# Kernel tuning notes

Hardware: AMD Instinct MI355X
Metric: run time of the kernel (lower is better)

The kernel has to match this reference:

```python
import jax, jax.numpy as jnp
import numpy as np

INPUTS = 6
GROUPS = 10
EPS = 1e-4

def setup_inputs() -> dict:
    key = jax.random.key(0)
    k1, k2, k3 = jax.random.split(key, 3)
    B = 1048576
    out = jax.random.normal(k1, (B, GROUPS * INPUTS), dtype=jnp.float32)
    # 10 Linear(6,1) layers stacked: W [10,6], b [10]
    bound = 1.0 / np.sqrt(INPUTS)
    W = jax.random.uniform(k2, (GROUPS, INPUTS), jnp.float32, -bound, bound)
    b = jax.random.uniform(k3, (GROUPS,), jnp.float32, -bound, bound)
    gamma = jnp.ones((GROUPS,), jnp.float32)
    beta = jnp.zeros((GROUPS,), jnp.float32)
    return {"out": out, "W": W, "b": b, "gamma": gamma, "beta": beta}

def reference(out, W, b, gamma, beta):
    B = out.shape[0]
    # grouped matmul: [B,10,6] x [10,6] -> [B,10]
    x = out[:, : GROUPS * INPUTS].reshape(B, GROUPS, INPUTS)
    y = jnp.einsum('bgi,gi->bg', x, W) + b  # [B,10]
    # BatchNorm1d training mode: batch mean, biased variance, eps=1e-4
    mean = jnp.mean(y, axis=0)
    var = jnp.mean((y - mean) ** 2, axis=0)
    y_hat = (y - mean) * jax.lax.rsqrt(var + EPS)
    return y_hat * gamma + beta
```

## Files before the change

kernel.cpp:

```cpp
#include <hip/hip_runtime.h>
#include <math.h>

#define GROUPS 10
#define INPUTS 6
#define COLS (GROUPS * INPUTS)
#define EPSV 1e-4f

#define TNT 64
#define TROWS 64
#define TF4 (TROWS * 15)
#define K1B 2560

#define NB1 2048
#define NT 256

__global__ __launch_bounds__(TNT) void k1_staged(
    const float* __restrict__ in,
    const float* __restrict__ Wp,
    const float* __restrict__ bp,
    float* __restrict__ y_out,
    float* __restrict__ partials,
    int ntiles)
{
    __shared__ float4 tile[TF4];
    const int tid = threadIdx.x;

    float Wr[COLS];
#pragma unroll
    for (int j = 0; j < COLS; ++j) Wr[j] = Wp[j];
    float br[GROUPS];
#pragma unroll
    for (int g = 0; g < GROUPS; ++g) br[g] = bp[g];

    float s[GROUPS], sq[GROUPS];
#pragma unroll
    for (int g = 0; g < GROUPS; ++g) { s[g] = 0.f; sq[g] = 0.f; }

    for (int t = blockIdx.x; t < ntiles; t += gridDim.x) {
        const float4* src = reinterpret_cast<const float4*>(in) + (size_t)t * TF4;

        __syncthreads();
#pragma unroll
        for (int j = 0; j < 15; ++j)
            tile[j * TNT + tid] = src[j * TNT + tid];
        __syncthreads();

        const float* x = reinterpret_cast<const float*>(&tile[tid * 15]);
        float y[GROUPS];
#pragma unroll
        for (int g = 0; g < GROUPS; ++g) {
            float acc = br[g];
#pragma unroll
            for (int i = 0; i < INPUTS; ++i)
                acc = fmaf(x[g * INPUTS + i], Wr[g * INPUTS + i], acc);
            y[g] = acc;
            s[g] += acc;
            sq[g] = fmaf(acc, acc, sq[g]);
        }

        const size_t r = (size_t)t * TROWS + tid;
        float2* yo = reinterpret_cast<float2*>(y_out + r * GROUPS);
#pragma unroll
        for (int j = 0; j < 5; ++j)
            yo[j] = make_float2(y[2 * j], y[2 * j + 1]);
    }

#pragma unroll
    for (int off = 32; off > 0; off >>= 1) {
#pragma unroll
        for (int g = 0; g < GROUPS; ++g) {
            s[g]  += __shfl_down(s[g],  off, 64);
            sq[g] += __shfl_down(sq[g], off, 64);
        }
    }
    if (tid == 0) {
        float* p = partials + (size_t)blockIdx.x * (2 * GROUPS);
#pragma unroll
        for (int g = 0; g < GROUPS; ++g) {
            p[g]          = s[g];
            p[GROUPS + g] = sq[g];
        }
    }
}

__global__ __launch_bounds__(NT) void k1_compute(
    const float* __restrict__ in, const float* __restrict__ Wp,
    const float* __restrict__ bp, float* __restrict__ y_out,
    float* __restrict__ partials, int B)
{
    const int tid = threadIdx.x;
    const int gid = blockIdx.x * NT + tid;
    const int stride = gridDim.x * NT;

    float Wr[COLS];
#pragma unroll
    for (int j = 0; j < COLS; ++j) Wr[j] = Wp[j];
    float br[GROUPS];
#pragma unroll
    for (int g = 0; g < GROUPS; ++g) br[g] = bp[g];

    float s[GROUPS], sq[GROUPS];
#pragma unroll
    for (int g = 0; g < GROUPS; ++g) { s[g] = 0.f; sq[g] = 0.f; }

    for (int r = gid; r < B; r += stride) {
        const float4* row4 = reinterpret_cast<const float4*>(in + (size_t)r * COLS);
        float4 v[15];
#pragma unroll
        for (int j = 0; j < 15; ++j) v[j] = row4[j];
        const float* x = reinterpret_cast<const float*>(v);
        float y[GROUPS];
#pragma unroll
        for (int g = 0; g < GROUPS; ++g) {
            float acc = br[g];
#pragma unroll
            for (int i = 0; i < INPUTS; ++i)
                acc = fmaf(x[g * INPUTS + i], Wr[g * INPUTS + i], acc);
            y[g] = acc;
            s[g] += acc;
            sq[g] = fmaf(acc, acc, sq[g]);
        }
        float2* yo = reinterpret_cast<float2*>(y_out + (size_t)r * GROUPS);
#pragma unroll
        for (int j = 0; j < 5; ++j) yo[j] = make_float2(y[2 * j], y[2 * j + 1]);
    }

#pragma unroll
    for (int off = 32; off > 0; off >>= 1) {
#pragma unroll
        for (int g = 0; g < GROUPS; ++g) {
            s[g]  += __shfl_down(s[g],  off, 64);
            sq[g] += __shfl_down(sq[g], off, 64);
        }
    }
    __shared__ float ls[NT / 64][2 * GROUPS];
    const int lane = tid & 63;
    const int wid  = tid >> 6;
    if (lane == 0) {
#pragma unroll
        for (int g = 0; g < GROUPS; ++g) {
            ls[wid][g]          = s[g];
            ls[wid][GROUPS + g] = sq[g];
        }
    }
    __syncthreads();
    if (tid < 2 * GROUPS) {
        float t = ls[0][tid] + ls[1][tid] + ls[2][tid] + ls[3][tid];
        partials[(size_t)blockIdx.x * (2 * GROUPS) + tid] = t;
    }
}

__global__ __launch_bounds__(NT) void k2_finalize(
    const float* __restrict__ partials, int nblocks,
    const float* __restrict__ gamma, const float* __restrict__ beta,
    float* __restrict__ ss, float invB)
{
    const int tid = threadIdx.x;
    float acc[2 * GROUPS];
#pragma unroll
    for (int j = 0; j < 2 * GROUPS; ++j) acc[j] = 0.f;
    for (int blk = tid; blk < nblocks; blk += NT) {
        const float* p = partials + (size_t)blk * (2 * GROUPS);
#pragma unroll
        for (int j = 0; j < 2 * GROUPS; ++j) acc[j] += p[j];
    }
#pragma unroll
    for (int off = 32; off > 0; off >>= 1) {
#pragma unroll
        for (int j = 0; j < 2 * GROUPS; ++j)
            acc[j] += __shfl_down(acc[j], off, 64);
    }
    __shared__ float ls[NT / 64][2 * GROUPS];
    const int lane = tid & 63;
    const int wid  = tid >> 6;
    if (lane == 0) {
#pragma unroll
        for (int j = 0; j < 2 * GROUPS; ++j) ls[wid][j] = acc[j];
    }
    __syncthreads();
    if (tid < GROUPS) {
        float sum  = ls[0][tid] + ls[1][tid] + ls[2][tid] + ls[3][tid];
        float sumq = ls[0][GROUPS + tid] + ls[1][GROUPS + tid] +
                     ls[2][GROUPS + tid] + ls[3][GROUPS + tid];
        float mean = sum * invB;
        float var  = sumq * invB - mean * mean;
        float sc   = gamma[tid] * rsqrtf(var + EPSV);
        ss[tid]          = sc;
        ss[GROUPS + tid] = beta[tid] - mean * sc;
    }
}

__global__ __launch_bounds__(NT) void k3_normalize(
    const float4* __restrict__ y4, const float* __restrict__ ss,
    float4* __restrict__ out4, int n4)
{
    __shared__ float sc[GROUPS], sh[GROUPS];
    if (threadIdx.x < GROUPS) {
        sc[threadIdx.x] = ss[threadIdx.x];
        sh[threadIdx.x] = ss[GROUPS + threadIdx.x];
    }
    __syncthreads();
    int gid = blockIdx.x * NT + threadIdx.x;
    int stride = gridDim.x * NT;
    for (int q = gid; q < n4; q += stride) {
        float4 v = y4[q];
        int g0 = (q * 4) % GROUPS;
        int g1 = g0 + 1; if (g1 >= GROUPS) g1 -= GROUPS;
        int g2 = g1 + 1; if (g2 >= GROUPS) g2 -= GROUPS;
        int g3 = g2 + 1; if (g3 >= GROUPS) g3 -= GROUPS;
        v.x = fmaf(v.x, sc[g0], sh[g0]);
        v.y = fmaf(v.y, sc[g1], sh[g1]);
        v.z = fmaf(v.z, sc[g2], sh[g2]);
        v.w = fmaf(v.w, sc[g3], sh[g3]);
        out4[q] = v;
    }
}

extern "C" void kernel_launch(void* const* d_in, const int* in_sizes, int n_in,
                              void* d_out, int out_size, void* d_ws, size_t ws_size,
                              hipStream_t stream)
{
    const float* in    = (const float*)d_in[0];
    const float* W     = (const float*)d_in[1];
    const float* bias  = (const float*)d_in[2];
    const float* gamma = (const float*)d_in[3];
    const float* beta  = (const float*)d_in[4];
    float* out = (float*)d_out;

    const int B = in_sizes[0] / COLS;
    float* ws = (float*)d_ws;

    const size_t yFloats = (size_t)B * GROUPS;

    const bool tiled = (B % TROWS) == 0;
    const int  nb1   = tiled ? ((B / TROWS < K1B) ? (B / TROWS) : K1B) : NB1;

    const size_t partFloats = (size_t)nb1 * 2 * GROUPS;
    const size_t needStore  = (yFloats + partFloats + 2 * GROUPS) * sizeof(float);

    if (ws_size >= needStore && ((size_t)B * GROUPS) % 4 == 0) {
        float* y_ws     = ws;
        float* partials = ws + yFloats;
        float* ss       = partials + partFloats;

        if (tiled) {
            k1_staged<<<nb1, TNT, 0, stream>>>(in, W, bias, y_ws, partials, B / TROWS);
        } else {
            k1_compute<<<nb1, NT, 0, stream>>>(in, W, bias, y_ws, partials, B);
        }
        k2_finalize<<<1, NT, 0, stream>>>(partials, nb1, gamma, beta, ss, 1.0f / (float)B);
        const int n4 = (B * GROUPS) / 4;
        k3_normalize<<<2048, NT, 0, stream>>>((const float4*)y_ws, ss, (float4*)out, n4);
    } else {
        float* partials = ws;
        float* ss       = partials + (size_t)NB1 * 2 * GROUPS;
        k1_compute<<<NB1, NT, 0, stream>>>(in, W, bias, ws, partials, B);
        k2_finalize<<<1, NT, 0, stream>>>(partials, NB1, gamma, beta, ss, 1.0f / (float)B);
    }
}
```

Measured before the change: 77.26 us.

## Store intermediate y as bf16 and fuse stats finalize into first kernel

The first kernel now writes the pre-normalization activations as packed bf16 instead of fp32, halving intermediate write and read traffic. The separate finalize kernel is replaced by a last-block-done pattern using an atomic ticket counter, so the final block reduces partials and computes scale/shift. The normalize kernel unpacks bf16 pairs and writes fp32 output. This trades accuracy (bf16 rounding of y before normalization) and adds a memset launch for the counter.

```diff
diff --git a/kernel.cpp b/kernel.cpp
--- a/kernel.cpp
+++ b/kernel.cpp
@@ -14,16 +14,30 @@
 #define NB1 2048
 #define NT 256
 
+__device__ inline unsigned bf16pair(float a, float b) {
+    unsigned ua = __float_as_uint(a);
+    unsigned ub = __float_as_uint(b);
+    ua += 0x7fffu + ((ua >> 16) & 1u);
+    ub += 0x7fffu + ((ub >> 16) & 1u);
+    return (ua >> 16) | (ub & 0xffff0000u);
+}
+
 __global__ __launch_bounds__(TNT) void k1_staged(
     const float* __restrict__ in,
     const float* __restrict__ Wp,
     const float* __restrict__ bp,
-    float* __restrict__ y_out,
+    const float* __restrict__ gamma,
+    const float* __restrict__ beta,
+    unsigned* __restrict__ y16,
     float* __restrict__ partials,
-    int ntiles)
+    float* __restrict__ ss,
+    unsigned* __restrict__ counter,
+    int ntiles, float invB)
 {
     __shared__ float4 tile[TF4];
+    __shared__ bool amLast;
     const int tid = threadIdx.x;
+    const int nblocks = gridDim.x;
 
     float Wr[COLS];
 #pragma unroll
@@ -36,7 +50,7 @@
 #pragma unroll
     for (int g = 0; g < GROUPS; ++g) { s[g] = 0.f; sq[g] = 0.f; }
 
-    for (int t = blockIdx.x; t < ntiles; t += gridDim.x) {
+    for (int t = blockIdx.x; t < ntiles; t += nblocks) {
         const float4* src = reinterpret_cast<const float4*>(in) + (size_t)t * TF4;
 
         __syncthreads();
@@ -59,10 +73,10 @@
         }
 
         const size_t r = (size_t)t * TROWS + tid;
-        float2* yo = reinterpret_cast<float2*>(y_out + r * GROUPS);
+        unsigned* yo = y16 + r * (GROUPS / 2);
 #pragma unroll
         for (int j = 0; j < 5; ++j)
-            yo[j] = make_float2(y[2 * j], y[2 * j + 1]);
+            yo[j] = bf16pair(y[2 * j], y[2 * j + 1]);
     }
 
 #pragma unroll
@@ -80,6 +94,78 @@
             p[g]          = s[g];
             p[GROUPS + g] = sq[g];
         }
+        __threadfence();
+        unsigned ticket = atomicAdd(counter, 1u);
+        amLast = (ticket == (unsigned)(nblocks - 1));
+    }
+    __syncthreads();
+
+    if (amLast) {
+        __threadfence();
+        float acc[2 * GROUPS];
+#pragma unroll
+        for (int j = 0; j < 2 * GROUPS; ++j) acc[j] = 0.f;
+        for (int b = tid; b < nblocks; b += TNT) {
+            const float* p = partials + (size_t)b * (2 * GROUPS);
+#pragma unroll
+            for (int j = 0; j < 2 * GROUPS; ++j) acc[j] += p[j];
+        }
+#pragma unroll
+        for (int off = 32; off > 0; off >>= 1) {
+#pragma unroll
+            for (int j = 0; j < 2 * GROUPS; ++j)
+                acc[j] += __shfl_down(acc[j], off, 64);
+        }
+        if (tid == 0) {
+#pragma unroll
+            for (int g = 0; g < GROUPS; ++g) {
+                float mean = acc[g] * invB;
+                float var  = acc[GROUPS + g] * invB - mean * mean;
+                float sc   = gamma[g] * rsqrtf(var + EPSV);
+                ss[g]          = sc;
+                ss[GROUPS + g] = beta[g] - mean * sc;
+            }
+        }
+    }
+}
+
+__global__ __launch_bounds__(NT) void k3_normalize_bf16(
+    const uint4* __restrict__ y8,
+    const float* __restrict__ ss,
+    float4* __restrict__ out4,
+    int n8)
+{
+    __shared__ float sc[GROUPS], sh[GROUPS];
+    if (threadIdx.x < GROUPS) {
+        sc[threadIdx.x] = ss[threadIdx.x];
+        sh[threadIdx.x] = ss[GROUPS + threadIdx.x];
+    }
+    __syncthreads();
+
+    int gid = blockIdx.x * NT + threadIdx.x;
+    int stride = gridDim.x * NT;
+    for (int q = gid; q < n8; q += stride) {
+        uint4 v = y8[q];
+        float e[8];
+        e[0] = __uint_as_float(v.x << 16);
+        e[1] = __uint_as_float(v.x & 0xffff0000u);
+        e[2] = __uint_as_float(v.y << 16);
+        e[3] = __uint_as_float(v.y & 0xffff0000u);
+        e[4] = __uint_as_float(v.z << 16);
+        e[5] = __uint_as_float(v.z & 0xffff0000u);
+        e[6] = __uint_as_float(v.w << 16);
+        e[7] = __uint_as_float(v.w & 0xffff0000u);
+
+        const int e0 = (q * 8) % GROUPS;
+        float r[8];
+#pragma unroll
+        for (int k = 0; k < 8; ++k) {
+            int g = e0 + k;
+            if (g >= GROUPS) g -= GROUPS;
+            r[k] = fmaf(e[k], sc[g], sh[g]);
+        }
+        out4[2 * q]     = make_float4(r[0], r[1], r[2], r[3]);
+        out4[2 * q + 1] = make_float4(r[4], r[5], r[6], r[7]);
     }
 }
 
@@ -228,33 +314,43 @@
     float* out = (float*)d_out;
 
     const int B = in_sizes[0] / COLS;
-    float* ws = (float*)d_ws;
-
-    const size_t yFloats = (size_t)B * GROUPS;
-
-    const bool tiled = (B % TROWS) == 0;
-    const int  nb1   = tiled ? ((B / TROWS < K1B) ? (B / TROWS) : K1B) : NB1;
-
-    const size_t partFloats = (size_t)nb1 * 2 * GROUPS;
-    const size_t needStore  = (yFloats + partFloats + 2 * GROUPS) * sizeof(float);
-
-    if (ws_size >= needStore && ((size_t)B * GROUPS) % 4 == 0) {
-        float* y_ws     = ws;
-        float* partials = ws + yFloats;
+    char* ws = (char*)d_ws;
+
+    if ((B % TROWS) == 0) {
+        const int ntiles = B / TROWS;
+        const int nb1    = (ntiles < K1B) ? ntiles : K1B;
+
+        const size_t yBytes    = (size_t)B * GROUPS * 2;
+        const size_t partBytes = (size_t)nb1 * 2 * GROUPS * sizeof(float);
+        size_t off = 0;
+        unsigned* y16   = (unsigned*)(ws + off); off += yBytes;
+        off = (off + 255) & ~(size_t)255;
+        float* partials = (float*)(ws + off);    off += partBytes;
+        float* ss       = (float*)(ws + off);    off += 2 * GROUPS * sizeof(float);
+        unsigned* ctr   = (unsigned*)(ws + off); off += sizeof(unsigned);
+
+        if (ws_size >= off) {
+            hipMemsetAsync(ctr, 0, sizeof(unsigned), stream);
+            k1_staged<<<nb1, TNT, 0, stream>>>(in, W, bias, gamma, beta,
+                                               y16, partials, ss, ctr,
+                                               ntiles, 1.0f / (float)B);
+            const int n8 = (B * GROUPS) / 8;
+            k3_normalize_bf16<<<2048, NT, 0, stream>>>(
+                (const uint4*)y16, ss, (float4*)out, n8);
+            return;
+        }
+    }
+
+    {
+        float* fws = (float*)d_ws;
+        const size_t yFloats    = (size_t)B * GROUPS;
+        const size_t partFloats = (size_t)NB1 * 2 * GROUPS;
+        float* y_ws     = fws;
+        float* partials = fws + yFloats;
         float* ss       = partials + partFloats;
-
-        if (tiled) {
-            k1_staged<<<nb1, TNT, 0, stream>>>(in, W, bias, y_ws, partials, B / TROWS);
-        } else {
-            k1_compute<<<nb1, NT, 0, stream>>>(in, W, bias, y_ws, partials, B);
-        }
-        k2_finalize<<<1, NT, 0, stream>>>(partials, nb1, gamma, beta, ss, 1.0f / (float)B);
+        k1_compute<<<NB1, NT, 0, stream>>>(in, W, bias, y_ws, partials, B);
+        k2_finalize<<<1, NT, 0, stream>>>(partials, NB1, gamma, beta, ss, 1.0f / (float)B);
         const int n4 = (B * GROUPS) / 4;
         k3_normalize<<<2048, NT, 0, stream>>>((const float4*)y_ws, ss, (float4*)out, n4);
-    } else {
-        float* partials = ws;
-        float* ss       = partials + (size_t)NB1 * 2 * GROUPS;
-        k1_compute<<<NB1, NT, 0, stream>>>(in, W, bias, ws, partials, B);
-        k2_finalize<<<1, NT, 0, stream>>>(partials, NB1, gamma, beta, ss, 1.0f / (float)B);
-    }
-}
+    }
+}
```

Result: slower. 201.6 us (+161.0%).
